# Kernel optimization log

Measured on AMD Instinct MI355X. Metric: run time of the kernel, lower is better.

Reference implementation:

```python
import jax, jax.numpy as jnp
import numpy as np

B, H, D = 32, 200000, 8

def setup_inputs() -> dict:
    key = jax.random.key(0)
    k1, k2, k3, k4 = jax.random.split(key, 4)
    col = jax.random.normal(k1, (B, D), dtype=jnp.float32)
    cen = jax.random.normal(k2, (B, H, D), dtype=jnp.float32)
    prc_h = jax.random.uniform(k3, (B, H, D), dtype=jnp.float32) + 0.5  # positive precisions
    hgt_h = jax.random.uniform(k4, (B, H), dtype=jnp.float32) * 0.01    # accumulated hill heights
    kbt = jnp.ones((B,), dtype=jnp.float32)
    wdt = jnp.ones((D,), dtype=jnp.float32)
    prc = 1.0 / (wdt * wdt)                  # buffer: 1/wdt^2
    hgt = jnp.asarray(0.01, dtype=jnp.float32)  # buffer: new hill base height
    gam = jnp.asarray(10.0, dtype=jnp.float32)  # buffer: bias factor gamma
    return {"col": col, "cen": cen, "prc_h": prc_h, "hgt_h": hgt_h,
            "kbt": kbt, "prc": prc, "hgt": hgt, "gam": gam}

def reference(col, cen, prc_h, hgt_h, kbt, prc, hgt, gam):
    # gaussian_potential: V_b = sum_h hgt[b,h] * exp(-0.5 * sum_d (cen-col)^2 * prc)
    r = cen - col[:, None, :]                     # (B,H,D)
    expo = -0.5 * jnp.sum(r * r * prc_h, axis=-1)  # (B,H)
    eng = jnp.sum(hgt_h * jnp.exp(expo), axis=1)   # (B,)
    # new_gaussian_wtmtd
    det = gam * kbt - kbt                          # (B,)
    new_hgt = hgt * jnp.exp(-eng / det)            # (B,) well-tempered height
    new_prc = jnp.broadcast_to(prc[None, :], (col.shape[0], prc.shape[0]))
    # add_gaussian: append new hill along hills dim
    cen_out = jnp.concatenate([cen, col[:, None, :]], axis=1)       # (B,H+1,D)
    prc_out = jnp.concatenate([prc_h, new_prc[:, None, :]], axis=1)  # (B,H+1,D)
    hgt_out = jnp.concatenate([hgt_h, new_hgt[:, None]], axis=1)     # (B,H+1)
    return cen_out, prc_out, hgt_out
```

## Files before the change

### kernel.cpp

```cpp
#include <hip/hip_runtime.h>


#define BB 32
#define HH 200000
#define DD 8
#define HPT 8
#define BLK 256

__global__ __launch_bounds__(BLK) void wtmtd_main(
    const float* __restrict__ col,
    const float* __restrict__ cen,
    const float* __restrict__ prc_h,
    const float* __restrict__ hgt_h,
    float* __restrict__ cen_out,
    float* __restrict__ prc_out,
    float* __restrict__ hgt_out,
    float* __restrict__ partials)
{
    const int b = blockIdx.y;

    const float4* colv = (const float4*)(col + (size_t)b * DD);
    const float4 c0 = colv[0];
    const float4 c1 = colv[1];

    const size_t inBase  = (size_t)b * HH;
    const size_t outBase = (size_t)b * (HH + 1);

    float local = 0.0f;
    const int h0 = blockIdx.x * (BLK * HPT) + threadIdx.x;

    #pragma unroll
    for (int i = 0; i < HPT; ++i) {
        const int h = h0 + i * BLK;
        if (h < HH) {
            const float4* cen4 = (const float4*)(cen   + (inBase + h) * DD);
            const float4* prc4 = (const float4*)(prc_h + (inBase + h) * DD);
            const float4 a0 = cen4[0];
            const float4 a1 = cen4[1];
            const float4 p0 = prc4[0];
            const float4 p1 = prc4[1];
            const float hh = hgt_h[inBase + h];

            float r, s;
            r = a0.x - c0.x; s  = r * r * p0.x;
            r = a0.y - c0.y; s += r * r * p0.y;
            r = a0.z - c0.z; s += r * r * p0.z;
            r = a0.w - c0.w; s += r * r * p0.w;
            r = a1.x - c1.x; s += r * r * p1.x;
            r = a1.y - c1.y; s += r * r * p1.y;
            r = a1.z - c1.z; s += r * r * p1.z;
            r = a1.w - c1.w; s += r * r * p1.w;

            local += hh * expf(-0.5f * s);

            float4* co = (float4*)(cen_out + (outBase + h) * DD);
            co[0] = a0; co[1] = a1;
            float4* po = (float4*)(prc_out + (outBase + h) * DD);
            po[0] = p0; po[1] = p1;
            hgt_out[outBase + h] = hh;
        }
    }

    #pragma unroll
    for (int off = 32; off > 0; off >>= 1)
        local += __shfl_down(local, off);

    __shared__ float sred[BLK / 64];
    const int lane = threadIdx.x & 63;
    const int wv   = threadIdx.x >> 6;
    if (lane == 0) sred[wv] = local;
    __syncthreads();
    if (threadIdx.x == 0) {
        float s = 0.0f;
        #pragma unroll
        for (int i = 0; i < BLK / 64; ++i) s += sred[i];
        partials[(size_t)b * gridDim.x + blockIdx.x] = s;
    }
}

__global__ __launch_bounds__(64) void wtmtd_fin(
    const float* __restrict__ partials, int nblk,
    const float* __restrict__ col,
    const float* __restrict__ kbt,
    const float* __restrict__ prc,
    const float* __restrict__ hgt,
    const float* __restrict__ gam,
    float* __restrict__ cen_out,
    float* __restrict__ prc_out,
    float* __restrict__ hgt_out)
{
    const int b = blockIdx.x;

    float s = 0.0f;
    for (int i = threadIdx.x; i < nblk; i += 64)
        s += partials[(size_t)b * nblk + i];
    #pragma unroll
    for (int off = 32; off > 0; off >>= 1)
        s += __shfl_down(s, off);
    s = __shfl(s, 0);

    const float det = kbt[b] * (gam[0] - 1.0f);
    const float new_hgt = hgt[0] * expf(-s / det);

    const size_t outBase = (size_t)b * (HH + 1);
    if (threadIdx.x < DD) {
        cen_out[(outBase + HH) * DD + threadIdx.x] = col[(size_t)b * DD + threadIdx.x];
        prc_out[(outBase + HH) * DD + threadIdx.x] = prc[threadIdx.x];
    }
    if (threadIdx.x == 0)
        hgt_out[outBase + HH] = new_hgt;
}

extern "C" void kernel_launch(void* const* d_in, const int* in_sizes, int n_in,
                              void* d_out, int out_size, void* d_ws, size_t ws_size,
                              hipStream_t stream) {
    const float* col   = (const float*)d_in[0];
    const float* cen   = (const float*)d_in[1];
    const float* prc_h = (const float*)d_in[2];
    const float* hgt_h = (const float*)d_in[3];
    const float* kbt   = (const float*)d_in[4];
    const float* prc   = (const float*)d_in[5];
    const float* hgt   = (const float*)d_in[6];
    const float* gam   = (const float*)d_in[7];

    float* cen_out = (float*)d_out;
    float* prc_out = cen_out + (size_t)BB * (HH + 1) * DD;
    float* hgt_out = prc_out + (size_t)BB * (HH + 1) * DD;

    float* partials = (float*)d_ws;

    const int nblk = (HH + BLK * HPT - 1) / (BLK * HPT);
    dim3 grid(nblk, BB);

    wtmtd_main<<<grid, BLK, 0, stream>>>(col, cen, prc_h, hgt_h,
                                         cen_out, prc_out, hgt_out, partials);
    wtmtd_fin<<<BB, 64, 0, stream>>>(partials, nblk, col, kbt, prc, hgt, gam,
                                     cen_out, prc_out, hgt_out);
}
```

Baseline: 186.0 us.

## Remap to one float4 per thread with lane-pair shuffle reduction

Each thread now handles one float4 (half a hill) instead of a full 8-float hill, so consecutive lanes touch consecutive 16-byte chunks. This makes the global loads and the copy-out stores fully coalesced. Adjacent lanes combine their half-sums with a shuffle, and only even lanes accumulate the weighted exponential. The hgt copy moves into a separate coalesced loop, and the fast __expf replaces expf, which may slightly change accuracy. A full-chunk fast path skips bounds checks.

```diff
diff --git a/kernel.cpp b/kernel.cpp
--- a/kernel.cpp
+++ b/kernel.cpp
@@ -4,8 +4,12 @@
 #define BB 32
 #define HH 200000
 #define DD 8
-#define HPT 8
 #define BLK 256
+#define IT 16
+#define CHUNK (BLK * IT)
+#define F4B (HH * 2)
+
+typedef float f32x4 __attribute__((ext_vector_type(4)));
 
 __global__ __launch_bounds__(BLK) void wtmtd_main(
     const float* __restrict__ col,
@@ -18,46 +22,65 @@
     float* __restrict__ partials)
 {
     const int b = blockIdx.y;
+    const int t = threadIdx.x;
 
-    const float4* colv = (const float4*)(col + (size_t)b * DD);
-    const float4 c0 = colv[0];
-    const float4 c1 = colv[1];
+    const size_t hIn  = (size_t)b * HH;
+    const size_t hOut = (size_t)b * (HH + 1);
 
-    const size_t inBase  = (size_t)b * HH;
-    const size_t outBase = (size_t)b * (HH + 1);
+    const f32x4* cen4 = (const f32x4*)cen   + (size_t)b * F4B;
+    const f32x4* prc4 = (const f32x4*)prc_h + (size_t)b * F4B;
+    f32x4* co = (f32x4*)cen_out + (size_t)b * (F4B + 2);
+    f32x4* po = (f32x4*)prc_out + (size_t)b * (F4B + 2);
+
+    const f32x4* colv = (const f32x4*)(col + (size_t)b * DD);
+    const f32x4 c_my  = colv[t & 1];
+    const float mask0 = (t & 1) ? 0.0f : 1.0f;
+
+    const int base  = blockIdx.x * CHUNK;
+    const int hbase = base >> 1;
+
+    #pragma unroll
+    for (int i = 0; i < IT / 2; ++i) {
+        const int h = hbase + i * BLK + t;
+        if (h < HH) hgt_out[hOut + h] = hgt_h[hIn + h];
+    }
 
     float local = 0.0f;
-    const int h0 = blockIdx.x * (BLK * HPT) + threadIdx.x;
+    const bool full = (base + CHUNK) <= F4B;
 
-    #pragma unroll
-    for (int i = 0; i < HPT; ++i) {
-        const int h = h0 + i * BLK;
-        if (h < HH) {
-            const float4* cen4 = (const float4*)(cen   + (inBase + h) * DD);
-            const float4* prc4 = (const float4*)(prc_h + (inBase + h) * DD);
-            const float4 a0 = cen4[0];
-            const float4 a1 = cen4[1];
-            const float4 p0 = prc4[0];
-            const float4 p1 = prc4[1];
-            const float hh = hgt_h[inBase + h];
+    if (full) {
+        #pragma unroll 4
+        for (int i = 0; i < IT; ++i) {
+            const int idx = base + i * BLK + t;
+            const f32x4 v = cen4[idx];
+            const f32x4 p = prc4[idx];
+            const float hh = hgt_h[hIn + (idx >> 1)];
 
-            float r, s;
-            r = a0.x - c0.x; s  = r * r * p0.x;
-            r = a0.y - c0.y; s += r * r * p0.y;
-            r = a0.z - c0.z; s += r * r * p0.z;
-            r = a0.w - c0.w; s += r * r * p0.w;
-            r = a1.x - c1.x; s += r * r * p1.x;
-            r = a1.y - c1.y; s += r * r * p1.y;
-            r = a1.z - c1.z; s += r * r * p1.z;
-            r = a1.w - c1.w; s += r * r * p1.w;
+            const f32x4 d = v - c_my;
+            float s = d.x*d.x*p.x + d.y*d.y*p.y + d.z*d.z*p.z + d.w*d.w*p.w;
+            s += __shfl_xor(s, 1);
+            local += mask0 * hh * __expf(-0.5f * s);
 
-            local += hh * expf(-0.5f * s);
+            co[idx] = v;
+            po[idx] = p;
+        }
+    } else {
+        #pragma unroll 4
+        for (int i = 0; i < IT; ++i) {
+            const int idx = base + i * BLK + t;
+            if (idx < F4B) {
+                const f32x4 v = cen4[idx];
+                const f32x4 p = prc4[idx];
+                const float hh = hgt_h[hIn + (idx >> 1)];
 
-            float4* co = (float4*)(cen_out + (outBase + h) * DD);
-            co[0] = a0; co[1] = a1;
-            float4* po = (float4*)(prc_out + (outBase + h) * DD);
-            po[0] = p0; po[1] = p1;
-            hgt_out[outBase + h] = hh;
+                const f32x4 d = v - c_my;
+                float s = d.x*d.x*p.x + d.y*d.y*p.y + d.z*d.z*p.z + d.w*d.w*p.w;
+                s += __shfl_xor(s, 1);
+                local += mask0 * hh * __expf(-0.5f * s);
+
+                co[idx] = v;
+                po[idx] = p;
+            }
         }
     }
 
@@ -66,11 +89,11 @@
         local += __shfl_down(local, off);
 
     __shared__ float sred[BLK / 64];
-    const int lane = threadIdx.x & 63;
-    const int wv   = threadIdx.x >> 6;
+    const int lane = t & 63;
+    const int wv   = t >> 6;
     if (lane == 0) sred[wv] = local;
     __syncthreads();
-    if (threadIdx.x == 0) {
+    if (t == 0) {
         float s = 0.0f;
         #pragma unroll
         for (int i = 0; i < BLK / 64; ++i) s += sred[i];
@@ -129,11 +152,11 @@
 
     float* partials = (float*)d_ws;
 
-    const int nblk = (HH + BLK * HPT - 1) / (BLK * HPT);
-    dim3 grid(nblk, BB);
+    const int nblkx = (F4B + CHUNK - 1) / CHUNK;
+    dim3 grid(nblkx, BB);
 
     wtmtd_main<<<grid, BLK, 0, stream>>>(col, cen, prc_h, hgt_h,
                                          cen_out, prc_out, hgt_out, partials);
-    wtmtd_fin<<<BB, 64, 0, stream>>>(partials, nblk, col, kbt, prc, hgt, gam,
+    wtmtd_fin<<<BB, 64, 0, stream>>>(partials, nblkx, col, kbt, prc, hgt, gam,
                                      cen_out, prc_out, hgt_out);
 }
```

New measurement: 187.1 us. No clear change (+0.6%).
